# Kernel optimization log

Measured on AMD Instinct MI355X. Metric: run time of the kernel, lower is better.

Reference implementation:

```python
import jax, jax.numpy as jnp
import numpy as np

VOL_SIZE = 1.0  # config.render.volume_size


def _make_grid(G, vol_size):
    # pytorch3d Volumes.get_coord_grid(world_coordinates=True): axis-aligned grid
    # centered at origin, spacing = voxel_size = vol_size/G, last dim is (x,y,z)
    # with x varying along W, y along H, z along D.
    m = (G - 1) / 2.0 * (vol_size / G)
    lin = jnp.linspace(-m, m, G, dtype=jnp.float32)
    zz, yy, xx = jnp.meshgrid(lin, lin, lin, indexing='ij')
    return jnp.stack([xx, yy, zz], axis=-1)  # [G,G,G,3]


def _grid_sample_3d(vol, grid):
    # vol: [N,C,D,H,W]; grid: [N,Dg,Hg,Wg,3] xyz in [-1,1].
    # Matches torch F.grid_sample(mode='bilinear', padding_mode='zeros', align_corners=False).
    N, C, D, H, W = vol.shape
    ix = ((grid[..., 0] + 1.0) * W - 1.0) * 0.5
    iy = ((grid[..., 1] + 1.0) * H - 1.0) * 0.5
    iz = ((grid[..., 2] + 1.0) * D - 1.0) * 0.5
    x0f, y0f, z0f = jnp.floor(ix), jnp.floor(iy), jnp.floor(iz)
    tx, ty, tz = ix - x0f, iy - y0f, iz - z0f
    x0, y0, z0 = x0f.astype(jnp.int32), y0f.astype(jnp.int32), z0f.astype(jnp.int32)

    def per_batch(v, z0, y0, x0, tx, ty, tz):
        # v: [C,D,H,W]; index/weight maps: [Dg,Hg,Wg]
        def corner(z, y, x):
            valid = (z >= 0) & (z < D) & (y >= 0) & (y < H) & (x >= 0) & (x < W)
            zc = jnp.clip(z, 0, D - 1)
            yc = jnp.clip(y, 0, H - 1)
            xc = jnp.clip(x, 0, W - 1)
            return v[:, zc, yc, xc] * valid[None]  # [C,Dg,Hg,Wg]
        z1, y1, x1 = z0 + 1, y0 + 1, x0 + 1
        acc = jnp.zeros((C,) + z0.shape, dtype=v.dtype)
        for zc, wz in ((z0, 1.0 - tz), (z1, tz)):
            for yc, wy in ((y0, 1.0 - ty), (y1, ty)):
                for xc, wx in ((x0, 1.0 - tx), (x1, tx)):
                    acc = acc + corner(zc, yc, xc) * (wz * wy * wx)[None]
        return acc

    return jax.vmap(per_batch)(vol, z0, y0, x0, tx, ty, tz)


def reference(voxels, camPoses_cv2, grid_size):
    B, t, C, D, H, W = voxels.shape
    G = grid_size
    m = (G - 1) / 2.0 * (VOL_SIZE / G)  # grid_coord_max
    grid_coord = _make_grid(G, VOL_SIZE)  # [G,G,G,3]

    # T = pose_0 @ pose_1^{-1}, per (B, t-1) pair
    pose0 = jnp.broadcast_to(camPoses_cv2[:, 0:1], (B, t - 1, 4, 4)).reshape(B * (t - 1), 4, 4)
    pose1 = camPoses_cv2[:, 1:].reshape(B * (t - 1), 4, 4)
    T = pose0 @ jnp.linalg.inv(pose1)

    # homogeneous transform of world grid points: cam = R @ p + trans
    pts = grid_coord.reshape(-1, 3)  # [N=G^3, 3]
    R, trans = T[:, :3, :3], T[:, :3, 3]
    cam = jnp.einsum('nij,pj->npi', R, pts) + trans[:, None, :]  # [B*(t-1), N, 3]
    sample_grid = (cam / m).reshape(B * (t - 1), D, H, W, 3)

    warped = _grid_sample_3d(voxels[:, 1:].reshape(B * (t - 1), C, D, H, W), sample_grid)
    out = jnp.concatenate([voxels[:, 0:1], warped.reshape(B, t - 1, C, D, H, W)], axis=1)
    return out


def setup_inputs() -> dict:
    key = jax.random.key(0)
    kv, ka, kt = jax.random.split(key, 3)
    B, t, C, G = 2, 5, 16, 64
    voxels = jax.random.normal(kv, (B, t, C, G, G, G), dtype=jnp.float32)
    # build valid SE(3)-ish camera poses (orthonormal rotation + small translation)
    A = jax.random.normal(ka, (B, t, 3, 3), dtype=jnp.float32)
    Q, _ = jnp.linalg.qr(A)
    det = jnp.linalg.det(Q)
    Q = Q * jnp.sign(det)[..., None, None]  # ensure det=+1
    trans = 0.2 * jax.random.normal(kt, (B, t, 3), dtype=jnp.float32)
    top = jnp.concatenate([Q, trans[..., None]], axis=-1)  # [B,t,3,4]
    bottom = jnp.broadcast_to(jnp.array([0.0, 0.0, 0.0, 1.0], jnp.float32), (B, t, 1, 4))
    camPoses_cv2 = jnp.concatenate([top, bottom], axis=-2)  # [B,t,4,4]
    return {"voxels": voxels, "camPoses_cv2": camPoses_cv2, "grid_size": G}
```

## Files before the change

kernel.cpp:

```cpp
#include <hip/hip_runtime.h>

#define G3_    (64 * 64 * 64)
#define CCH    16
#define TT     5
#define LSTRIDE 17
#define MAXZ   15
#define BUF    4096
#define NWARP  4096
#define NCOPY  8192
#define NBLK   (NWARP + NCOPY)

__global__ __launch_bounds__(256) void fused_kernel(const float* __restrict__ vox,
                                                    const float* __restrict__ cam,
                                                    float* __restrict__ out)
{
    __shared__ float lds[2 * BUF];
    const int tid = threadIdx.x;

    const int bid  = blockIdx.x;
    const int sbid = (bid & 7) * (NBLK / 8) + (bid >> 3);
    const int w3   = sbid / 3;
    const int r3   = sbid - w3 * 3;

    if (r3 != 0) {
        int cid = (w3 << 1) + (r3 - 1);
        int t4  = cid * 256 + tid;
        int b   = t4 >> 20;
        int rr  = t4 & ((1 << 20) - 1);
        size_t base = (size_t)(b * TT) * CCH * G3_;
        const float4* s = (const float4*)(vox + base);
        float4* d = (float4*)(out + base);
        d[rr] = s[rr];
        return;
    }

    const int n  = w3 >> 9;
    const int t6 = w3 & 511;
    const int ox = (t6 & 7) << 3;
    const int oy = ((t6 >> 3) & 7) << 3;
    const int oz = (t6 >> 6) << 3;
    const int b  = n >> 2, j = n & 3;

    const float* p0 = cam + (size_t)(b * TT) * 16;
    const float* p1 = cam + (size_t)(b * TT + j + 1) * 16;
    float a00 = p0[0], a01 = p0[1], a02 = p0[2],  at0 = p0[3];
    float a10 = p0[4], a11 = p0[5], a12 = p0[6],  at1 = p0[7];
    float a20 = p0[8], a21 = p0[9], a22 = p0[10], at2 = p0[11];
    float b00 = p1[0], b01 = p1[1], b02 = p1[2],  bt0 = p1[3];
    float b10 = p1[4], b11 = p1[5], b12 = p1[6],  bt1 = p1[7];
    float b20 = p1[8], b21 = p1[9], b22 = p1[10], bt2 = p1[11];
    float R00 = a00*b00 + a01*b01 + a02*b02;
    float R01 = a00*b10 + a01*b11 + a02*b12;
    float R02 = a00*b20 + a01*b21 + a02*b22;
    float R10 = a10*b00 + a11*b01 + a12*b02;
    float R11 = a10*b10 + a11*b11 + a12*b12;
    float R12 = a10*b20 + a11*b21 + a12*b22;
    float R20 = a20*b00 + a21*b01 + a22*b02;
    float R21 = a20*b10 + a21*b11 + a22*b12;
    float R22 = a20*b20 + a21*b21 + a22*b22;
    float trx = at0 - (R00*bt0 + R01*bt1 + R02*bt2);
    float try_= at1 - (R10*bt0 + R11*bt1 + R12*bt2);
    float trz = at2 - (R20*bt0 + R21*bt1 + R22*bt2);

    const float S  = 1.0f / 64.0f;
    const float SC = 32.0f / 0.4921875f;
    const float ax = SC * R00 * S, bx = SC * R01 * S, cx = SC * R02 * S;
    const float ay = SC * R10 * S, by = SC * R11 * S, cy = SC * R12 * S;
    const float az = SC * R20 * S, bz = SC * R21 * S, cz = SC * R22 * S;
    const float kx = -31.5f * (ax + bx + cx) + SC * trx + 31.5f;
    const float ky = -31.5f * (ay + by + cy) + SC * try_ + 31.5f;
    const float kz = -31.5f * (az + bz + cz) + SC * trz + 31.5f;

    float x0a = ax * ox, x0b = ax * (ox + 7);
    float x1a = bx * oy, x1b = bx * (oy + 7);
    float x2a = cx * oz, x2b = cx * (oz + 7);
    float min_ix = kx + fminf(x0a, x0b) + fminf(x1a, x1b) + fminf(x2a, x2b);
    float max_ix = kx + fmaxf(x0a, x0b) + fmaxf(x1a, x1b) + fmaxf(x2a, x2b);
    float y0a = ay * ox, y0b = ay * (ox + 7);
    float y1a = by * oy, y1b = by * (oy + 7);
    float y2a = cy * oz, y2b = cy * (oz + 7);
    float min_iy = ky + fminf(y0a, y0b) + fminf(y1a, y1b) + fminf(y2a, y2b);
    float max_iy = ky + fmaxf(y0a, y0b) + fmaxf(y1a, y1b) + fmaxf(y2a, y2b);
    float z0a = az * ox, z0b = az * (ox + 7);
    float z1a = bz * oy, z1b = bz * (oy + 7);
    float z2a = cz * oz, z2b = cz * (oz + 7);
    float min_iz = kz + fminf(z0a, z0b) + fminf(z1a, z1b) + fminf(z2a, z2b);
    float max_iz = kz + fmaxf(z0a, z0b) + fmaxf(z1a, z1b) + fmaxf(z2a, z2b);

    int xlo = min(max((int)floorf(min_ix), 0), 63);
    int xhi = min(max((int)floorf(max_ix) + 1, 0), 63);
    int ylo = min(max((int)floorf(min_iy), 0), 63);
    int yhi = min(max((int)floorf(max_iy) + 1, 0), 63);
    int zlo = min(max((int)floorf(min_iz), 0), 63);
    int zhi = min(max((int)floorf(max_iz) + 1, 0), 63);
    const int xlo_e = xlo & ~1;
    const int sxe = xhi - xlo_e + 1;
    const int sy  = yhi - ylo + 1;
    const int sz  = zhi - zlo + 1;
    const int lstep = sy * LSTRIDE;

    float wx0[2], wx1[2], wy0[2], wy1[2], wz0[2], wz1[2];
    int base0[2], base1[2], soff[2];
    #pragma unroll
    for (int k = 0; k < 2; ++k) {
        int o  = tid + (k << 8);
        int gx = ox + (o & 7);
        int gy = oy + ((o >> 3) & 7);
        int gz = oz + (o >> 6);
        float ix = kx + ax * gx + bx * gy + cx * gz;
        float iy = ky + ay * gx + by * gy + cy * gz;
        float iz = kz + az * gx + bz * gy + cz * gz;
        float fx = floorf(ix), fy = floorf(iy), fz = floorf(iz);
        float tx = ix - fx, ty = iy - fy, tz = iz - fz;
        int X0 = (int)fx, Y0 = (int)fy, Z0 = (int)fz;

        float w0 = ((unsigned)X0 < 64u) ? (1.0f - tx) : 0.0f;
        float w1 = ((unsigned)(X0 + 1) < 64u) ? tx : 0.0f;
        int rxu = X0 - xlo_e;
        wx0[k] = (rxu < 0) ? w1 : w0;
        wx1[k] = (rxu < 0) ? 0.0f : w1;
        int rx0 = min(max(rxu, 0), sxe - 1);

        w0 = ((unsigned)Y0 < 64u) ? (1.0f - ty) : 0.0f;
        w1 = ((unsigned)(Y0 + 1) < 64u) ? ty : 0.0f;
        int ryu = Y0 - ylo;
        wy0[k] = (ryu < 0) ? w1 : w0;
        wy1[k] = (ryu < 0) ? 0.0f : w1;
        int ry0 = min(max(ryu, 0), sy - 1);

        wz0[k] = ((unsigned)Z0 < 64u) ? (1.0f - tz) : 0.0f;
        wz1[k] = ((unsigned)(Z0 + 1) < 64u) ? tz : 0.0f;
        int rz0 = min(max(Z0     - zlo, 0), sz - 1);
        int rz1 = min(max(Z0 + 1 - zlo, 0), sz - 1);

        base0[k] = rz0 * lstep + ry0 * LSTRIDE + rx0;
        base1[k] = rz1 * lstep + ry0 * LSTRIDE + rx0;
        soff[k]  = (gz << 12) + (gy << 6) + gx;
    }

    const size_t fb = (size_t)((b * TT + j + 1) * CCH) * G3_;
    const float* vbase = vox + fb;
    float* obase = out + fb;

    const int lane8 = tid & 7;
    const int row16 = (tid >> 3) & 15;
    const int zh    = tid >> 7;
    const int xe    = xlo_e + (lane8 << 1);
    const bool actS = (xe <= xhi) && (row16 < sy);
    const int grow  = (zlo << 12) + ((ylo + row16) << 6) + xe;
    const int lrow  = row16 * LSTRIDE + (lane8 << 1);

    #pragma unroll
    for (int i = 0; i < 32; ++i) lds[tid + i * 256] = 0.0f;
    __syncthreads();

    if (actS) {
        const float2* gp = (const float2*)(vbase + grow);
        #pragma unroll
        for (int k = 0; k < 8; ++k) {
            int zz = (k << 1) + zh;
            if (zz < sz) {
                float2 v = gp[(size_t)zz << 11];
                float* wp = lds + lrow + zz * lstep;
                wp[0] = v.x;
                wp[1] = v.y;
            }
        }
    }
    __syncthreads();

    for (int c = 0; c < CCH; ++c) {
        float2 stg[8];
        const bool pre = (c + 1 < CCH);
        if (pre && actS) {
            const float2* gp = (const float2*)(vbase + (size_t)(c + 1) * G3_ + grow);
            #pragma unroll
            for (int k = 0; k < 8; ++k) {
                int zz = (k << 1) + zh;
                if (zz < sz) stg[k] = gp[(size_t)zz << 11];
            }
        }

        const float* buf = lds + (c & 1) * BUF;
        float* op = obase + (size_t)c * G3_;
        #pragma unroll
        for (int k = 0; k < 2; ++k) {
            const float* pz0 = buf + base0[k];
            const float* pz1 = buf + base1[k];
            float v000 = pz0[0],  v001 = pz0[1];
            float v010 = pz0[17], v011 = pz0[18];
            float v100 = pz1[0],  v101 = pz1[1];
            float v110 = pz1[17], v111 = pz1[18];
            float t00 = v000 * wx0[k] + v001 * wx1[k];
            float t01 = v010 * wx0[k] + v011 * wx1[k];
            float t10 = v100 * wx0[k] + v101 * wx1[k];
            float t11 = v110 * wx0[k] + v111 * wx1[k];
            float u0  = t00 * wy0[k] + t01 * wy1[k];
            float u1  = t10 * wy0[k] + t11 * wy1[k];
            op[soff[k]] = u0 * wz0[k] + u1 * wz1[k];
        }

        if (pre) {
            float* wbuf = lds + ((c + 1) & 1) * BUF;
            if (actS) {
                #pragma unroll
                for (int k = 0; k < 8; ++k) {
                    int zz = (k << 1) + zh;
                    if (zz < sz) {
                        float* wp = wbuf + lrow + zz * lstep;
                        wp[0] = stg[k].x;
                        wp[1] = stg[k].y;
                    }
                }
            }
            __syncthreads();
        }
    }
}

extern "C" void kernel_launch(void* const* d_in, const int* in_sizes, int n_in,
                              void* d_out, int out_size, void* d_ws, size_t ws_size,
                              hipStream_t stream)
{
    const float* vox = (const float*)d_in[0];
    const float* cam = (const float*)d_in[1];
    float* out = (float*)d_out;
    (void)d_ws;

    hipLaunchKernelGGL(fused_kernel, dim3(NBLK), dim3(256), 0, stream, vox, cam, out);
}
```

Baseline: 398.9 us.

## Split warp blocks across channel groups and single-buffer the LDS tile

Each warp block now handles 4 channels instead of all 16, which gives four times as many warp blocks. The copy and warp blocks are re-interleaved two to one. The LDS shrinks to a single buffer, and an extra barrier is added before each refill. The first load is issued before the zero-fill so their latency overlaps. The aim is more parallelism and occupancy, paid for by redoing the pose and weight setup in every channel group and by an extra sync per channel.

```diff
diff --git a/kernel.cpp b/kernel.cpp
--- a/kernel.cpp
+++ b/kernel.cpp
@@ -4,9 +4,9 @@
 #define CCH    16
 #define TT     5
 #define LSTRIDE 17
-#define MAXZ   15
 #define BUF    4096
-#define NWARP  4096
+#define NCHB   4
+#define NWARP  (4096 * (CCH / NCHB))
 #define NCOPY  8192
 #define NBLK   (NWARP + NCOPY)
 
@@ -14,19 +14,18 @@
                                                     const float* __restrict__ cam,
                                                     float* __restrict__ out)
 {
-    __shared__ float lds[2 * BUF];
+    __shared__ float lds[BUF];
     const int tid = threadIdx.x;
 
     const int bid  = blockIdx.x;
     const int sbid = (bid & 7) * (NBLK / 8) + (bid >> 3);
-    const int w3   = sbid / 3;
-    const int r3   = sbid - w3 * 3;
-
-    if (r3 != 0) {
-        int cid = (w3 << 1) + (r3 - 1);
-        int t4  = cid * 256 + tid;
-        int b   = t4 >> 20;
-        int rr  = t4 & ((1 << 20) - 1);
+    const int q3   = sbid / 3;
+    const int r3   = sbid - q3 * 3;
+
+    if (r3 == 2) {
+        int t4 = q3 * 256 + tid;
+        int b  = t4 >> 20;
+        int rr = t4 & ((1 << 20) - 1);
         size_t base = (size_t)(b * TT) * CCH * G3_;
         const float4* s = (const float4*)(vox + base);
         float4* d = (float4*)(out + base);
@@ -34,12 +33,15 @@
         return;
     }
 
-    const int n  = w3 >> 9;
-    const int t6 = w3 & 511;
-    const int ox = (t6 & 7) << 3;
-    const int oy = ((t6 >> 3) & 7) << 3;
-    const int oz = (t6 >> 6) << 3;
-    const int b  = n >> 2, j = n & 3;
+    const int wid = q3 * 2 + r3;
+    const int cg  = wid >> 12;
+    const int t9  = wid & 4095;
+    const int n   = t9 >> 9;
+    const int t6  = t9 & 511;
+    const int ox  = (t6 & 7) << 3;
+    const int oy  = ((t6 >> 3) & 7) << 3;
+    const int oz  = (t6 >> 6) << 3;
+    const int b   = n >> 2, j = n & 3;
 
     const float* p0 = cam + (size_t)(b * TT) * 16;
     const float* p1 = cam + (size_t)(b * TT + j + 1) * 16;
@@ -138,7 +140,7 @@
         soff[k]  = (gz << 12) + (gy << 6) + gx;
     }
 
-    const size_t fb = (size_t)((b * TT + j + 1) * CCH) * G3_;
+    const size_t fb = ((size_t)(b * TT + j + 1) * CCH + cg * NCHB) * G3_;
     const float* vbase = vox + fb;
     float* obase = out + fb;
 
@@ -150,30 +152,36 @@
     const int grow  = (zlo << 12) + ((ylo + row16) << 6) + xe;
     const int lrow  = row16 * LSTRIDE + (lane8 << 1);
 
-    #pragma unroll
-    for (int i = 0; i < 32; ++i) lds[tid + i * 256] = 0.0f;
-    __syncthreads();
+    float2 stg[8];
 
     if (actS) {
         const float2* gp = (const float2*)(vbase + grow);
         #pragma unroll
         for (int k = 0; k < 8; ++k) {
             int zz = (k << 1) + zh;
+            if (zz < sz) stg[k] = gp[(size_t)zz << 11];
+        }
+    }
+    #pragma unroll
+    for (int i = 0; i < 16; ++i) lds[tid + i * 256] = 0.0f;
+    __syncthreads();
+    if (actS) {
+        #pragma unroll
+        for (int k = 0; k < 8; ++k) {
+            int zz = (k << 1) + zh;
             if (zz < sz) {
-                float2 v = gp[(size_t)zz << 11];
                 float* wp = lds + lrow + zz * lstep;
-                wp[0] = v.x;
-                wp[1] = v.y;
+                wp[0] = stg[k].x;
+                wp[1] = stg[k].y;
             }
         }
     }
     __syncthreads();
 
-    for (int c = 0; c < CCH; ++c) {
-        float2 stg[8];
-        const bool pre = (c + 1 < CCH);
+    for (int cc = 0; cc < NCHB; ++cc) {
+        const bool pre = (cc + 1 < NCHB);
         if (pre && actS) {
-            const float2* gp = (const float2*)(vbase + (size_t)(c + 1) * G3_ + grow);
+            const float2* gp = (const float2*)(vbase + (size_t)(cc + 1) * G3_ + grow);
             #pragma unroll
             for (int k = 0; k < 8; ++k) {
                 int zz = (k << 1) + zh;
@@ -181,12 +189,11 @@
             }
         }
 
-        const float* buf = lds + (c & 1) * BUF;
-        float* op = obase + (size_t)c * G3_;
+        float* op = obase + (size_t)cc * G3_;
         #pragma unroll
         for (int k = 0; k < 2; ++k) {
-            const float* pz0 = buf + base0[k];
-            const float* pz1 = buf + base1[k];
+            const float* pz0 = lds + base0[k];
+            const float* pz1 = lds + base1[k];
             float v000 = pz0[0],  v001 = pz0[1];
             float v010 = pz0[17], v011 = pz0[18];
             float v100 = pz1[0],  v101 = pz1[1];
@@ -201,13 +208,13 @@
         }
 
         if (pre) {
-            float* wbuf = lds + ((c + 1) & 1) * BUF;
+            __syncthreads();
             if (actS) {
                 #pragma unroll
                 for (int k = 0; k < 8; ++k) {
                     int zz = (k << 1) + zh;
                     if (zz < sz) {
-                        float* wp = wbuf + lrow + zz * lstep;
+                        float* wp = lds + lrow + zz * lstep;
                         wp[0] = stg[k].x;
                         wp[1] = stg[k].y;
                     }
```

Measured after the change: 357.7 us. 1.12x faster.
